# Performance work log

Hardware: AMD Instinct MI355X
Metric: run time of the kernel (lower is better)

The kernel has to match this reference:

```python
import jax, jax.numpy as jnp
import numpy as np

N_QUBITS = 8  # 2**8 == hidden_dim == 256


def setup_inputs() -> dict:
    key = jax.random.key(0)
    ks = jax.random.split(key, 6)
    B, H, F = 131072, 256, 512
    s = lambda fan: 1.0 / np.sqrt(fan)
    return {
        "x": jax.random.normal(ks[0], (B, N_QUBITS), jnp.float32),
        "W1": jax.random.normal(ks[1], (N_QUBITS, H), jnp.float32) * s(N_QUBITS),
        "b1": jnp.zeros((H,), jnp.float32),
        "W2": jax.random.normal(ks[2], (H, H), jnp.float32) * s(H),
        "b2": jnp.zeros((H,), jnp.float32),
        "W3": jax.random.normal(ks[3], (H, H), jnp.float32) * s(H),
        "b3": jnp.zeros((H,), jnp.float32),
        "W4": jax.random.normal(ks[4], (H, F), jnp.float32) * s(H),
        "b4": jnp.zeros((F,), jnp.float32),
    }


def _quantum_state(enc):
    # Ry(theta_i) on qubit i from |0...0>: product state, amplitudes are
    # kron_i [cos(theta_i/2), sin(theta_i/2)] (real). Qubit 0 = most significant.
    half = enc[:, :N_QUBITS] * (jnp.pi / 2)  # theta/2 = enc*pi/2
    amps = jnp.stack([jnp.cos(half), jnp.sin(half)], axis=-1)  # [B, n, 2]
    B = enc.shape[0]
    state = jnp.ones((B, 1), enc.dtype)
    for i in range(N_QUBITS):  # fixed small structural loop
        state = (state[:, :, None] * amps[:, i, None, :]).reshape(B, -1)
    return state  # [B, 2**n]


def reference(x, W1, b1, W2, b2, W3, b3, W4, b4):
    h = jax.nn.relu(x @ W1 + b1)
    enc = jax.nn.relu(h @ W2 + b2)           # [B, 256]
    state = _quantum_state(enc)              # [B, 256]
    f = jax.nn.relu(state @ W3 + b3)
    return f @ W4 + b4                       # [B, 512]
```

## Files before the change

kernel.cpp:

```cpp
#include <hip/hip_runtime.h>
#include <hip/hip_bf16.h>

typedef short s8v __attribute__((ext_vector_type(8)));
typedef float f4v __attribute__((ext_vector_type(4)));
typedef unsigned short u16;
typedef unsigned int u32;

#define PI_HALF 1.57079632679489662f

__global__ void prep_kernel(const float* __restrict__ W1,
                            const float* __restrict__ W2,
                            const float* __restrict__ W3,
                            const float* __restrict__ W4,
                            u16* __restrict__ w3f,
                            u16* __restrict__ w4f,
                            float* __restrict__ w1t,
                            float* __restrict__ w2c) {
  int i = blockIdx.x * 256 + threadIdx.x;
  if (i < 65536) {
    int j = i & 7, lane = (i >> 3) & 63, kk = (i >> 9) & 7, ntg = i >> 12;
    int k = kk * 32 + (lane >> 4) * 8 + j;
    int n = ntg * 16 + (lane & 15);
    __hip_bfloat16 v = __float2bfloat16(W3[k * 256 + n]);
    w3f[i] = *(u16*)&v;
  } else if (i < 65536 + 131072) {
    int t = i - 65536;
    int j = t & 7, lane = (t >> 3) & 63, kk = (t >> 9) & 7, ntg = t >> 12;
    int k = kk * 32 + (lane >> 4) * 8 + j;
    int n = ntg * 16 + (lane & 15);
    __hip_bfloat16 v = __float2bfloat16(W4[k * 512 + n]);
    w4f[t] = *(u16*)&v;
  } else if (i < 65536 + 131072 + 2048) {
    int t = i - (65536 + 131072);
    int k = t >> 3, j = t & 7;
    w1t[t] = W1[j * 256 + k];
  } else if (i < 65536 + 131072 + 4096) {
    int t = i - (65536 + 131072 + 2048);
    int k = t >> 3, q = t & 7;
    w2c[t] = W2[k * 256 + q];
  }
}

__global__ __launch_bounds__(512, 2)
void fused_kernel(const float* __restrict__ x,
                  const float* __restrict__ b1v,
                  const float* __restrict__ b2v,
                  const float* __restrict__ b3v,
                  const float* __restrict__ b4v,
                  const u16* __restrict__ w3f,
                  const u16* __restrict__ w4f,
                  const float* __restrict__ w1t,
                  const float* __restrict__ w2c,
                  float* __restrict__ out, int B) {
  __shared__ alignas(16) u16 st[128 * 256];
  const int tid = threadIdx.x;
  const int row0 = blockIdx.x * 128;

  if (tid < 128) {
    const int r = row0 + tid;
    float xv[8];
    if (r < B) {
      const float4* xp = (const float4*)(x + (size_t)r * 8);
      float4 a = xp[0], b = xp[1];
      xv[0] = a.x; xv[1] = a.y; xv[2] = a.z; xv[3] = a.w;
      xv[4] = b.x; xv[5] = b.y; xv[6] = b.z; xv[7] = b.w;
    } else {
#pragma unroll
      for (int j = 0; j < 8; j++) xv[j] = 0.f;
    }
    float e[8];
#pragma unroll
    for (int q = 0; q < 8; q++) e[q] = b2v[q];
#pragma unroll 4
    for (int k = 0; k < 256; k++) {
      const float4* wp = (const float4*)(w1t + k * 8);
      float4 wa = wp[0], wb = wp[1];
      float h = b1v[k];
      h = fmaf(xv[0], wa.x, h); h = fmaf(xv[1], wa.y, h);
      h = fmaf(xv[2], wa.z, h); h = fmaf(xv[3], wa.w, h);
      h = fmaf(xv[4], wb.x, h); h = fmaf(xv[5], wb.y, h);
      h = fmaf(xv[6], wb.z, h); h = fmaf(xv[7], wb.w, h);
      h = fmaxf(h, 0.f);
      const float4* w2p = (const float4*)(w2c + k * 8);
      float4 ya = w2p[0], yb = w2p[1];
      e[0] = fmaf(h, ya.x, e[0]); e[1] = fmaf(h, ya.y, e[1]);
      e[2] = fmaf(h, ya.z, e[2]); e[3] = fmaf(h, ya.w, e[3]);
      e[4] = fmaf(h, yb.x, e[4]); e[5] = fmaf(h, yb.y, e[5]);
      e[6] = fmaf(h, yb.z, e[6]); e[7] = fmaf(h, yb.w, e[7]);
    }
    float cc[8], ss[8];
#pragma unroll
    for (int q = 0; q < 8; q++) {
      float ang = fmaxf(e[q], 0.f) * PI_HALF;
      ss[q] = __sinf(ang);
      cc[q] = __cosf(ang);
    }
    float A16[16], L16[16];
    {
      float t4[4], t8[8];
      t4[0] = cc[0] * cc[1]; t4[1] = cc[0] * ss[1];
      t4[2] = ss[0] * cc[1]; t4[3] = ss[0] * ss[1];
#pragma unroll
      for (int j = 0; j < 4; j++) { t8[2*j] = t4[j] * cc[2]; t8[2*j+1] = t4[j] * ss[2]; }
#pragma unroll
      for (int j = 0; j < 8; j++) { A16[2*j] = t8[j] * cc[3]; A16[2*j+1] = t8[j] * ss[3]; }
      t4[0] = cc[4] * cc[5]; t4[1] = cc[4] * ss[5];
      t4[2] = ss[4] * cc[5]; t4[3] = ss[4] * ss[5];
#pragma unroll
      for (int j = 0; j < 4; j++) { t8[2*j] = t4[j] * cc[6]; t8[2*j+1] = t4[j] * ss[6]; }
#pragma unroll
      for (int j = 0; j < 8; j++) { L16[2*j] = t8[j] * cc[7]; L16[2*j+1] = t8[j] * ss[7]; }
    }
#pragma unroll
    for (int g = 0; g < 32; g++) {
      float ah = A16[g >> 1];
      const int lo0 = (g & 1) << 3;
      union { u16 h8[8]; uint4 u4; } pk;
#pragma unroll
      for (int j = 0; j < 8; j++) {
        __hip_bfloat16 bv = __float2bfloat16(ah * L16[lo0 + j]);
        pk.h8[j] = *(u16*)&bv;
      }
      u32 byte = (u32)(tid * 512 + g * 16) ^ (u32)((tid & 7) << 4);
      *(uint4*)((char*)st + byte) = pk.u4;
    }
  }
  __syncthreads();

  const int lane = tid & 63;
  const int wid  = tid >> 6;
  const int wm   = wid >> 2;
  const int wn   = wid & 3;
  const int lr   = lane & 15;
  const int lg   = lane >> 4;
  const int m0   = wm * 64;

  f4v accA[4][4];
#pragma unroll
  for (int nt = 0; nt < 4; nt++)
#pragma unroll
    for (int mt = 0; mt < 4; mt++) accA[nt][mt] = (f4v){0.f, 0.f, 0.f, 0.f};

  for (int kk = 0; kk < 8; kk++) {
    s8v a[4];
#pragma unroll
    for (int mt = 0; mt < 4; mt++) {
      int row = m0 + mt * 16 + lr;
      u32 byte = (u32)(row * 512 + kk * 64 + lg * 16) ^ (u32)((row & 7) << 4);
      a[mt] = *(const s8v*)((const char*)st + byte);
    }
#pragma unroll
    for (int nt = 0; nt < 4; nt++) {
      int ntg = wn * 4 + nt;
      s8v b = ((const s8v*)w3f)[(ntg * 8 + kk) * 64 + lane];
#pragma unroll
      for (int mt = 0; mt < 4; mt++)
        accA[nt][mt] = __builtin_amdgcn_mfma_f32_16x16x32_bf16(a[mt], b, accA[nt][mt], 0, 0, 0);
    }
  }
  __syncthreads();

#pragma unroll
  for (int nt = 0; nt < 4; nt++) {
    int col = wn * 64 + nt * 16 + lr;
    float bias = b3v[col];
#pragma unroll
    for (int mt = 0; mt < 4; mt++) {
#pragma unroll
      for (int i = 0; i < 4; i++) {
        int row = m0 + mt * 16 + lg * 4 + i;
        float v = fmaxf(accA[nt][mt][i] + bias, 0.f);
        __hip_bfloat16 bv = __float2bfloat16(v);
        u32 byte = (u32)(row * 512 + col * 2) ^ (u32)((row & 7) << 4);
        *(u16*)((char*)st + byte) = *(u16*)&bv;
      }
    }
  }
  __syncthreads();

#pragma unroll 1
  for (int nh = 0; nh < 2; nh++) {
    const int nbase = wn * 128 + nh * 64;
    f4v accB[4][4];
#pragma unroll
    for (int nt = 0; nt < 4; nt++)
#pragma unroll
      for (int mt = 0; mt < 4; mt++) accB[nt][mt] = (f4v){0.f, 0.f, 0.f, 0.f};

    for (int kk = 0; kk < 8; kk++) {
      s8v a[4];
#pragma unroll
      for (int mt = 0; mt < 4; mt++) {
        int row = m0 + mt * 16 + lr;
        u32 byte = (u32)(row * 512 + kk * 64 + lg * 16) ^ (u32)((row & 7) << 4);
        a[mt] = *(const s8v*)((const char*)st + byte);
      }
#pragma unroll
      for (int nt = 0; nt < 4; nt++) {
        int ntg = (nbase >> 4) + nt;
        s8v b = ((const s8v*)w4f)[(ntg * 8 + kk) * 64 + lane];
#pragma unroll
        for (int mt = 0; mt < 4; mt++)
          accB[nt][mt] = __builtin_amdgcn_mfma_f32_16x16x32_bf16(a[mt], b, accB[nt][mt], 0, 0, 0);
      }
    }
#pragma unroll
    for (int nt = 0; nt < 4; nt++) {
      int col = nbase + nt * 16 + lr;
      float bias = b4v[col];
#pragma unroll
      for (int mt = 0; mt < 4; mt++) {
        int rowg = row0 + m0 + mt * 16 + lg * 4;
        if (rowg + 3 < B) {
          float* op = out + (size_t)rowg * 512 + col;
          op[0]    = accB[nt][mt][0] + bias;
          op[512]  = accB[nt][mt][1] + bias;
          op[1024] = accB[nt][mt][2] + bias;
          op[1536] = accB[nt][mt][3] + bias;
        } else {
#pragma unroll
          for (int i = 0; i < 4; i++)
            if (rowg + i < B) out[(size_t)(rowg + i) * 512 + col] = accB[nt][mt][i] + bias;
        }
      }
    }
  }
}

extern "C" void kernel_launch(void* const* d_in, const int* in_sizes, int n_in,
                              void* d_out, int out_size, void* d_ws, size_t ws_size,
                              hipStream_t stream) {
  const float* x  = (const float*)d_in[0];
  const float* W1 = (const float*)d_in[1];
  const float* b1 = (const float*)d_in[2];
  const float* W2 = (const float*)d_in[3];
  const float* b2 = (const float*)d_in[4];
  const float* W3 = (const float*)d_in[5];
  const float* b3 = (const float*)d_in[6];
  const float* W4 = (const float*)d_in[7];
  const float* b4 = (const float*)d_in[8];
  float* out = (float*)d_out;
  const int B = in_sizes[0] / 8;

  u16*   w3f = (u16*)d_ws;
  u16*   w4f = (u16*)((char*)d_ws + 131072);
  float* w1t = (float*)((char*)d_ws + 131072 + 262144);
  float* w2c = (float*)((char*)d_ws + 131072 + 262144 + 8192);

  prep_kernel<<<784, 256, 0, stream>>>(W1, W2, W3, W4, w3f, w4f, w1t, w2c);

  const int grid = (B + 127) / 128;
  fused_kernel<<<grid, 512, 0, stream>>>(x, b1, b2, b3, b4, w3f, w4f, w1t, w2c, out, B);
}
```

Baseline: 215.3 us.

## Split angle MLP into separate kernel and spread state build across all threads

Moves the per-row 8→256→8 MLP and the sin/cos evaluation out of the fused kernel into a standalone angle kernel that writes 16 floats per row to workspace. Previously only 128 of 512 threads did this serial work while the rest waited. The GEMM kernel now uses 64-row tiles so each of its 512 threads builds a slice of one row's 256-entry product state. This removes the idle-thread phase and halves LDS use per block, at the cost of an extra launch, a round trip of 8 MB through global memory, and half the MFMA work per wave in the GEMM.

```diff
diff --git a/kernel.cpp b/kernel.cpp
--- a/kernel.cpp
+++ b/kernel.cpp
@@ -41,87 +41,104 @@
   }
 }
 
+__global__ void angle_kernel(const float* __restrict__ x,
+                             const float* __restrict__ b1v,
+                             const float* __restrict__ b2v,
+                             const float* __restrict__ w1t,
+                             const float* __restrict__ w2c,
+                             float* __restrict__ cs, int B) {
+  const int r = blockIdx.x * 256 + threadIdx.x;
+  if (r >= B) return;
+  float xv[8];
+  {
+    const float4* xp = (const float4*)(x + (size_t)r * 8);
+    float4 a = xp[0], b = xp[1];
+    xv[0] = a.x; xv[1] = a.y; xv[2] = a.z; xv[3] = a.w;
+    xv[4] = b.x; xv[5] = b.y; xv[6] = b.z; xv[7] = b.w;
+  }
+  float e[8];
+#pragma unroll
+  for (int q = 0; q < 8; q++) e[q] = b2v[q];
+#pragma unroll 4
+  for (int k = 0; k < 256; k++) {
+    const float4* wp = (const float4*)(w1t + k * 8);
+    float4 wa = wp[0], wb = wp[1];
+    float h = b1v[k];
+    h = fmaf(xv[0], wa.x, h); h = fmaf(xv[1], wa.y, h);
+    h = fmaf(xv[2], wa.z, h); h = fmaf(xv[3], wa.w, h);
+    h = fmaf(xv[4], wb.x, h); h = fmaf(xv[5], wb.y, h);
+    h = fmaf(xv[6], wb.z, h); h = fmaf(xv[7], wb.w, h);
+    h = fmaxf(h, 0.f);
+    const float4* w2p = (const float4*)(w2c + k * 8);
+    float4 ya = w2p[0], yb = w2p[1];
+    e[0] = fmaf(h, ya.x, e[0]); e[1] = fmaf(h, ya.y, e[1]);
+    e[2] = fmaf(h, ya.z, e[2]); e[3] = fmaf(h, ya.w, e[3]);
+    e[4] = fmaf(h, yb.x, e[4]); e[5] = fmaf(h, yb.y, e[5]);
+    e[6] = fmaf(h, yb.z, e[6]); e[7] = fmaf(h, yb.w, e[7]);
+  }
+  float cc[8], ss[8];
+#pragma unroll
+  for (int q = 0; q < 8; q++) {
+    float ang = fmaxf(e[q], 0.f) * PI_HALF;
+    ss[q] = __sinf(ang);
+    cc[q] = __cosf(ang);
+  }
+  float4* op = (float4*)(cs + (size_t)r * 16);
+  op[0] = (float4){cc[0], cc[1], cc[2], cc[3]};
+  op[1] = (float4){cc[4], cc[5], cc[6], cc[7]};
+  op[2] = (float4){ss[0], ss[1], ss[2], ss[3]};
+  op[3] = (float4){ss[4], ss[5], ss[6], ss[7]};
+}
+
 __global__ __launch_bounds__(512, 2)
-void fused_kernel(const float* __restrict__ x,
-                  const float* __restrict__ b1v,
-                  const float* __restrict__ b2v,
-                  const float* __restrict__ b3v,
-                  const float* __restrict__ b4v,
-                  const u16* __restrict__ w3f,
-                  const u16* __restrict__ w4f,
-                  const float* __restrict__ w1t,
-                  const float* __restrict__ w2c,
-                  float* __restrict__ out, int B) {
-  __shared__ alignas(16) u16 st[128 * 256];
+void gemm_kernel(const float* __restrict__ cs,
+                 const float* __restrict__ b3v,
+                 const float* __restrict__ b4v,
+                 const u16* __restrict__ w3f,
+                 const u16* __restrict__ w4f,
+                 float* __restrict__ out, int B) {
+  __shared__ alignas(16) u16 st[64 * 256];
   const int tid = threadIdx.x;
-  const int row0 = blockIdx.x * 128;
-
-  if (tid < 128) {
-    const int r = row0 + tid;
-    float xv[8];
+  const int row0 = blockIdx.x * 64;
+
+  {
+    const int rl = tid >> 3;
+    const int s  = tid & 7;
+    const int r  = row0 + rl;
+    float4 ca, cb, sa, sb;
     if (r < B) {
-      const float4* xp = (const float4*)(x + (size_t)r * 8);
-      float4 a = xp[0], b = xp[1];
-      xv[0] = a.x; xv[1] = a.y; xv[2] = a.z; xv[3] = a.w;
-      xv[4] = b.x; xv[5] = b.y; xv[6] = b.z; xv[7] = b.w;
+      const float4* ip = (const float4*)(cs + (size_t)r * 16);
+      ca = ip[0]; cb = ip[1]; sa = ip[2]; sb = ip[3];
     } else {
-#pragma unroll
-      for (int j = 0; j < 8; j++) xv[j] = 0.f;
-    }
-    float e[8];
-#pragma unroll
-    for (int q = 0; q < 8; q++) e[q] = b2v[q];
-#pragma unroll 4
-    for (int k = 0; k < 256; k++) {
-      const float4* wp = (const float4*)(w1t + k * 8);
-      float4 wa = wp[0], wb = wp[1];
-      float h = b1v[k];
-      h = fmaf(xv[0], wa.x, h); h = fmaf(xv[1], wa.y, h);
-      h = fmaf(xv[2], wa.z, h); h = fmaf(xv[3], wa.w, h);
-      h = fmaf(xv[4], wb.x, h); h = fmaf(xv[5], wb.y, h);
-      h = fmaf(xv[6], wb.z, h); h = fmaf(xv[7], wb.w, h);
-      h = fmaxf(h, 0.f);
-      const float4* w2p = (const float4*)(w2c + k * 8);
-      float4 ya = w2p[0], yb = w2p[1];
-      e[0] = fmaf(h, ya.x, e[0]); e[1] = fmaf(h, ya.y, e[1]);
-      e[2] = fmaf(h, ya.z, e[2]); e[3] = fmaf(h, ya.w, e[3]);
-      e[4] = fmaf(h, yb.x, e[4]); e[5] = fmaf(h, yb.y, e[5]);
-      e[6] = fmaf(h, yb.z, e[6]); e[7] = fmaf(h, yb.w, e[7]);
-    }
-    float cc[8], ss[8];
-#pragma unroll
-    for (int q = 0; q < 8; q++) {
-      float ang = fmaxf(e[q], 0.f) * PI_HALF;
-      ss[q] = __sinf(ang);
-      cc[q] = __cosf(ang);
-    }
-    float A16[16], L16[16];
+      ca = cb = sa = sb = (float4){0.f, 0.f, 0.f, 0.f};
+    }
+    float q0 = (s & 4) ? sa.x : ca.x;
+    float q1 = (s & 2) ? sa.y : ca.y;
+    float q2 = (s & 1) ? sa.z : ca.z;
+    float prefix = q0 * q1 * q2;
+    float A2_0 = prefix * ca.w;
+    float A2_1 = prefix * sa.w;
+    float L16[16];
     {
       float t4[4], t8[8];
-      t4[0] = cc[0] * cc[1]; t4[1] = cc[0] * ss[1];
-      t4[2] = ss[0] * cc[1]; t4[3] = ss[0] * ss[1];
-#pragma unroll
-      for (int j = 0; j < 4; j++) { t8[2*j] = t4[j] * cc[2]; t8[2*j+1] = t4[j] * ss[2]; }
-#pragma unroll
-      for (int j = 0; j < 8; j++) { A16[2*j] = t8[j] * cc[3]; A16[2*j+1] = t8[j] * ss[3]; }
-      t4[0] = cc[4] * cc[5]; t4[1] = cc[4] * ss[5];
-      t4[2] = ss[4] * cc[5]; t4[3] = ss[4] * ss[5];
-#pragma unroll
-      for (int j = 0; j < 4; j++) { t8[2*j] = t4[j] * cc[6]; t8[2*j+1] = t4[j] * ss[6]; }
-#pragma unroll
-      for (int j = 0; j < 8; j++) { L16[2*j] = t8[j] * cc[7]; L16[2*j+1] = t8[j] * ss[7]; }
-    }
-#pragma unroll
-    for (int g = 0; g < 32; g++) {
-      float ah = A16[g >> 1];
-      const int lo0 = (g & 1) << 3;
+      t4[0] = cb.x * cb.y; t4[1] = cb.x * sb.y;
+      t4[2] = sb.x * cb.y; t4[3] = sb.x * sb.y;
+#pragma unroll
+      for (int j = 0; j < 4; j++) { t8[2*j] = t4[j] * cb.z; t8[2*j+1] = t4[j] * sb.z; }
+#pragma unroll
+      for (int j = 0; j < 8; j++) { L16[2*j] = t8[j] * cb.w; L16[2*j+1] = t8[j] * sb.w; }
+    }
+#pragma unroll
+    for (int it = 0; it < 4; it++) {
+      float ah = (it < 2) ? A2_0 : A2_1;
+      const int lo0 = (it & 1) << 3;
       union { u16 h8[8]; uint4 u4; } pk;
 #pragma unroll
       for (int j = 0; j < 8; j++) {
         __hip_bfloat16 bv = __float2bfloat16(ah * L16[lo0 + j]);
         pk.h8[j] = *(u16*)&bv;
       }
-      u32 byte = (u32)(tid * 512 + g * 16) ^ (u32)((tid & 7) << 4);
+      u32 byte = (u32)(rl * 512 + (s * 4 + it) * 16) ^ (u32)((rl & 7) << 4);
       *(uint4*)((char*)st + byte) = pk.u4;
     }
   }
@@ -133,18 +150,18 @@
   const int wn   = wid & 3;
   const int lr   = lane & 15;
   const int lg   = lane >> 4;
-  const int m0   = wm * 64;
-
-  f4v accA[4][4];
+  const int m0   = wm * 32;
+
+  f4v accA[4][2];
 #pragma unroll
   for (int nt = 0; nt < 4; nt++)
 #pragma unroll
-    for (int mt = 0; mt < 4; mt++) accA[nt][mt] = (f4v){0.f, 0.f, 0.f, 0.f};
+    for (int mt = 0; mt < 2; mt++) accA[nt][mt] = (f4v){0.f, 0.f, 0.f, 0.f};
 
   for (int kk = 0; kk < 8; kk++) {
-    s8v a[4];
-#pragma unroll
-    for (int mt = 0; mt < 4; mt++) {
+    s8v a[2];
+#pragma unroll
+    for (int mt = 0; mt < 2; mt++) {
       int row = m0 + mt * 16 + lr;
       u32 byte = (u32)(row * 512 + kk * 64 + lg * 16) ^ (u32)((row & 7) << 4);
       a[mt] = *(const s8v*)((const char*)st + byte);
@@ -154,7 +171,7 @@
       int ntg = wn * 4 + nt;
       s8v b = ((const s8v*)w3f)[(ntg * 8 + kk) * 64 + lane];
 #pragma unroll
-      for (int mt = 0; mt < 4; mt++)
+      for (int mt = 0; mt < 2; mt++)
         accA[nt][mt] = __builtin_amdgcn_mfma_f32_16x16x32_bf16(a[mt], b, accA[nt][mt], 0, 0, 0);
     }
   }
@@ -165,7 +182,7 @@
     int col = wn * 64 + nt * 16 + lr;
     float bias = b3v[col];
 #pragma unroll
-    for (int mt = 0; mt < 4; mt++) {
+    for (int mt = 0; mt < 2; mt++) {
 #pragma unroll
       for (int i = 0; i < 4; i++) {
         int row = m0 + mt * 16 + lg * 4 + i;
@@ -181,16 +198,16 @@
 #pragma unroll 1
   for (int nh = 0; nh < 2; nh++) {
     const int nbase = wn * 128 + nh * 64;
-    f4v accB[4][4];
+    f4v accB[4][2];
 #pragma unroll
     for (int nt = 0; nt < 4; nt++)
 #pragma unroll
-      for (int mt = 0; mt < 4; mt++) accB[nt][mt] = (f4v){0.f, 0.f, 0.f, 0.f};
+      for (int mt = 0; mt < 2; mt++) accB[nt][mt] = (f4v){0.f, 0.f, 0.f, 0.f};
 
     for (int kk = 0; kk < 8; kk++) {
-      s8v a[4];
-#pragma unroll
-      for (int mt = 0; mt < 4; mt++) {
+      s8v a[2];
+#pragma unroll
+      for (int mt = 0; mt < 2; mt++) {
         int row = m0 + mt * 16 + lr;
         u32 byte = (u32)(row * 512 + kk * 64 + lg * 16) ^ (u32)((row & 7) << 4);
         a[mt] = *(const s8v*)((const char*)st + byte);
@@ -200,7 +217,7 @@
         int ntg = (nbase >> 4) + nt;
         s8v b = ((const s8v*)w4f)[(ntg * 8 + kk) * 64 + lane];
 #pragma unroll
-        for (int mt = 0; mt < 4; mt++)
+        for (int mt = 0; mt < 2; mt++)
           accB[nt][mt] = __builtin_amdgcn_mfma_f32_16x16x32_bf16(a[mt], b, accB[nt][mt], 0, 0, 0);
       }
     }
@@ -209,7 +226,7 @@
       int col = nbase + nt * 16 + lr;
       float bias = b4v[col];
 #pragma unroll
-      for (int mt = 0; mt < 4; mt++) {
+      for (int mt = 0; mt < 2; mt++) {
         int rowg = row0 + m0 + mt * 16 + lg * 4;
         if (rowg + 3 < B) {
           float* op = out + (size_t)rowg * 512 + col;
@@ -246,9 +263,9 @@
   u16*   w4f = (u16*)((char*)d_ws + 131072);
   float* w1t = (float*)((char*)d_ws + 131072 + 262144);
   float* w2c = (float*)((char*)d_ws + 131072 + 262144 + 8192);
+  float* cs  = (float*)((char*)d_ws + 131072 + 262144 + 16384);
 
   prep_kernel<<<784, 256, 0, stream>>>(W1, W2, W3, W4, w3f, w4f, w1t, w2c);
-
-  const int grid = (B + 127) / 128;
-  fused_kernel<<<grid, 512, 0, stream>>>(x, b1, b2, b3, b4, w3f, w4f, w1t, w2c, out, B);
-}
+  angle_kernel<<<(B + 255) / 256, 256, 0, stream>>>(x, b1, b2, w1t, w2c, cs, B);
+  gemm_kernel<<<(B + 63) / 64, 512, 0, stream>>>(cs, b3, b4, w3f, w4f, out, B);
+}
```

After: 201.3 us. 6.5% less time.
